# Kernel optimization log

Hardware: AMD Instinct MI355X
Metric: run time of the kernel (lower is better)

The kernel has to match this reference:

```python
import jax, jax.numpy as jnp
import numpy as np

HIDDEN = 2048
NUM_HEADS = 16
HEAD_DIM = HIDDEN // NUM_HEADS


def setup_inputs() -> dict:
    key = jax.random.key(0)
    k1, k2, k3 = jax.random.split(key, 3)
    hidden_states = jax.random.normal(k1, (4, 2048, HIDDEN), dtype=jnp.float32)
    # torch Linear weight is (out, in); y = x @ W.T. Store transposed (in, out).
    w_qkv = jax.random.normal(k2, (HIDDEN, 3 * HIDDEN), dtype=jnp.float32) * (HIDDEN ** -0.5)
    w_o = jax.random.normal(k3, (HIDDEN, HIDDEN), dtype=jnp.float32) * (HIDDEN ** -0.5)
    return {"hidden_states": hidden_states, "w_qkv": w_qkv, "w_o": w_o}


def reference(hidden_states, w_qkv, w_o):
    B, S, _ = hidden_states.shape
    qkv = hidden_states @ w_qkv  # (B, S, 3*HIDDEN)
    # Faithful to torch .view: row-major reshape straight to (B, H, S, 3*head_dim)
    qkv = qkv.reshape(B, NUM_HEADS, S, 3 * HEAD_DIM)
    q, k, v = jnp.split(qkv, 3, axis=-1)  # each (B, H, S, head_dim)
    scores = jnp.einsum('bhsd,bhtd->bhst', q, k) / (HEAD_DIM ** 0.5)
    probs = jax.nn.softmax(scores, axis=-1)
    attn = jnp.einsum('bhst,bhtd->bhsd', probs, v)  # (B, H, S, head_dim)
    # Faithful to torch .reshape(B, S, hidden) without transpose
    attn = attn.reshape(B, S, HIDDEN)
    return attn @ w_o
```

## Files before the change

kernel.cpp:

```cpp
#include <hip/hip_runtime.h>
#include <stdint.h>

#define DEVINL __device__ __forceinline__

typedef __attribute__((ext_vector_type(8))) __bf16 bf16x8;
typedef __attribute__((ext_vector_type(4))) float f32x4;
typedef __attribute__((ext_vector_type(16))) float f32x16;

static constexpr int HID  = 2048;
static constexpr int NQ   = 6144;
static constexpr int SEQ  = 2048;
static constexpr int NB   = 4;
static constexpr int MTOT = NB * SEQ;

DEVINL unsigned short f2bf(float f) {
  union { float f; uint32_t u; } x; x.f = f;
  uint32_t r = x.u + 0x7fffu + ((x.u >> 16) & 1u);
  return (unsigned short)(r >> 16);
}

typedef const __attribute__((address_space(1))) void gvoid_t;
typedef __attribute__((address_space(3))) void svoid_t;

DEVINL void gload_lds16(const void* g, void* s) {
  __builtin_amdgcn_global_load_lds((gvoid_t*)(uintptr_t)g,
                                   (svoid_t*)(uint32_t)(uintptr_t)s,
                                   16, 0, 0);
}


__global__ void k_cvt(const float* __restrict__ in, unsigned short* __restrict__ out, int n4) {
  int i = blockIdx.x * blockDim.x + threadIdx.x;
  if (i >= n4) return;
  float4 v = ((const float4*)in)[i];
  ushort4 o;
  o.x = f2bf(v.x); o.y = f2bf(v.y); o.z = f2bf(v.z); o.w = f2bf(v.w);
  ((ushort4*)out)[i] = o;
}

__global__ void k_transpose_cvt(const float* __restrict__ in, unsigned short* __restrict__ out,
                                int R, int C) {
  __shared__ float tile[32][33];
  int c0 = blockIdx.x * 32, r0 = blockIdx.y * 32;
  int tx = threadIdx.x & 31, ty = threadIdx.x >> 5;
  #pragma unroll
  for (int i = 0; i < 32; i += 8)
    tile[ty + i][tx] = in[(size_t)(r0 + ty + i) * C + (c0 + tx)];
  __syncthreads();
  #pragma unroll
  for (int i = 0; i < 32; i += 8)
    out[(size_t)(c0 + ty + i) * R + (r0 + tx)] = f2bf(tile[tx][ty + i]);
}


template <int OUT_BF16>
__global__ __launch_bounds__(256, 2) void k_gemm2(const unsigned short* __restrict__ A,
                                                  const unsigned short* __restrict__ BT,
                                                  void* __restrict__ Cout,
                                                  int M, int N, int K) {
  __shared__ unsigned short As[256 * 64];
  __shared__ unsigned short Bs[128 * 64];
  const int tid = threadIdx.x;
  const int w = tid >> 6, l = tid & 63;
  const int lane16 = l & 15, lgrp = l >> 4;
  const int bn = blockIdx.x, bm = blockIdx.y;
  const int srow = l >> 3;
  const int gslot = (l & 7) ^ (l >> 3);

  f32x4 acc[4][8] = {};

  for (int k0 = 0; k0 < K; k0 += 64) {
    #pragma unroll
    for (int i = 0; i < 8; ++i) {
      const int chunk = i * 4 + w;
      const int row = chunk * 8 + srow;
      gload_lds16(A + (size_t)(bm * 256 + row) * K + k0 + gslot * 8, As + chunk * 512);
    }
    #pragma unroll
    for (int i = 0; i < 4; ++i) {
      const int chunk = i * 4 + w;
      const int row = chunk * 8 + srow;
      gload_lds16(BT + (size_t)(bn * 128 + row) * K + k0 + gslot * 8, Bs + chunk * 512);
    }
    __syncthreads();

    #pragma unroll
    for (int kk = 0; kk < 2; ++kk) {
      bf16x8 af[4], bfr[8];
      #pragma unroll
      for (int mf = 0; mf < 4; ++mf) {
        const int row = w * 64 + mf * 16 + lane16;
        af[mf] = *(const bf16x8*)(As + row * 64 + (((kk * 4 + lgrp) ^ (row & 7)) * 8));
      }
      #pragma unroll
      for (int nf = 0; nf < 8; ++nf) {
        const int row = nf * 16 + lane16;
        bfr[nf] = *(const bf16x8*)(Bs + row * 64 + (((kk * 4 + lgrp) ^ (row & 7)) * 8));
      }
      #pragma unroll
      for (int mf = 0; mf < 4; ++mf)
        #pragma unroll
        for (int nf = 0; nf < 8; ++nf)
          acc[mf][nf] = __builtin_amdgcn_mfma_f32_16x16x32_bf16(af[mf], bfr[nf], acc[mf][nf], 0, 0, 0);
    }
    __syncthreads();
  }

  const size_t row0 = (size_t)bm * 256 + w * 64;
  const int col0 = bn * 128;
  #pragma unroll
  for (int mf = 0; mf < 4; ++mf) {
    #pragma unroll
    for (int nf = 0; nf < 8; ++nf) {
      const int col = col0 + nf * 16 + lane16;
      #pragma unroll
      for (int r = 0; r < 4; ++r) {
        const size_t row = row0 + mf * 16 + lgrp * 4 + r;
        if (OUT_BF16)
          ((unsigned short*)Cout)[row * N + col] = f2bf(acc[mf][nf][r]);
        else
          ((float*)Cout)[row * N + col] = acc[mf][nf][r];
      }
    }
  }
}

__global__ void k_build_vt(const unsigned short* __restrict__ QKV, unsigned short* __restrict__ Vt) {
  const int head = blockIdx.y;
  const int s_rel = blockIdx.x;
  const int b = head >> 4, h = head & 15;
  const int d = threadIdx.x;
  const unsigned short* src = QKV + (size_t)(b * SEQ + h * 128 + s_rel) * NQ + 256 + d;
  unsigned short vals[16];
  #pragma unroll
  for (int c1 = 0; c1 < 16; ++c1) vals[c1] = src[c1 * 384];
  unsigned short* dst = Vt + ((size_t)head * 128 + d) * SEQ + s_rel * 16;
  #pragma unroll
  for (int c1 = 0; c1 < 16; ++c1) dst[c1] = vals[c1];
}

__global__ __launch_bounds__(256, 2) void k_attn(const unsigned short* __restrict__ QKV,
                                                 const unsigned short* __restrict__ Vt,
                                                 unsigned short* __restrict__ ATT) {
  __shared__ unsigned short Ks[2][64 * 128];
  __shared__ unsigned short Vs[2][128 * 64];
  const int tid = threadIdx.x, w = tid >> 6, l = tid & 63;
  const int l32 = l & 31, hi = l >> 5;
  const int qt = blockIdx.x, head = blockIdx.y;
  const int b = head >> 4, h = head & 15;
  const float scale = 0.08838834764831845f;
  const float THR = 8.0f / 0.08838834764831845f;
  const int base_row = b * SEQ + h * 128;

  const int s = qt * 128 + w * 32 + l32;
  bf16x8 qf[8];
  {
    const unsigned short* qrow = QKV + (size_t)(base_row + (s >> 4)) * NQ + (s & 15) * 384;
    #pragma unroll
    for (int dsl = 0; dsl < 8; ++dsl)
      qf[dsl] = *(const bf16x8*)(qrow + dsl * 16 + hi * 8);
  }

  f32x16 oacc[4] = {};
  float mrun = -1e30f, lrun = 0.0f;

  #define STAGE_KV(bb, kv0)                                                              \
    {                                                                                    \
      _Pragma("unroll")                                                                  \
      for (int i = 0; i < 4; ++i) {                                                      \
        const int chunk = i * 4 + w;                                                     \
        const int r = chunk * 4 + (l >> 4);                                              \
        const int colsw = ((l & 15) ^ (r & 15)) * 8;                                     \
        gload_lds16(QKV + (size_t)(base_row + ((kv0) >> 4) + (r >> 4)) * NQ              \
                        + (r & 15) * 384 + 128 + colsw,                                  \
                    &Ks[bb][chunk * 512]);                                               \
      }                                                                                  \
      _Pragma("unroll")                                                                  \
      for (int i = 0; i < 4; ++i) {                                                      \
        const int chunk = i * 4 + w;                                                     \
        const int dr = chunk * 8 + (l >> 3);                                             \
        const int colsw = ((l & 7) ^ (dr & 7)) * 8;                                      \
        gload_lds16(Vt + ((size_t)head * 128 + dr) * SEQ + (kv0) + colsw,                \
                    &Vs[bb][chunk * 512]);                                               \
      }                                                                                  \
    }

  STAGE_KV(0, 0);
  __syncthreads();

  int buf = 0;
  for (int kv0 = 0; kv0 < SEQ; kv0 += 64) {
    if (kv0 + 64 < SEQ) STAGE_KV(buf ^ 1, kv0 + 64);

    f32x16 sacc[2] = {};
    __builtin_amdgcn_s_setprio(1);
    #pragma unroll
    for (int kvf = 0; kvf < 2; ++kvf) {
      const int row = kvf * 32 + l32;
      const unsigned short* kbase = &Ks[buf][row * 128];
      const int rs = (row & 15) << 3;
      #pragma unroll
      for (int dsl = 0; dsl < 8; ++dsl) {
        bf16x8 kf = *(const bf16x8*)(kbase + ((dsl * 16 + hi * 8) ^ rs));
        sacc[kvf] = __builtin_amdgcn_mfma_f32_32x32x16_bf16(kf, qf[dsl], sacc[kvf], 0, 0, 0);
      }
    }
    __builtin_amdgcn_s_setprio(0);

    float mx[16];
    #pragma unroll
    for (int r = 0; r < 16; ++r) mx[r] = fmaxf(sacc[0][r], sacc[1][r]);
    #pragma unroll
    for (int st = 8; st >= 1; st >>= 1)
      #pragma unroll
      for (int r = 0; r < st; ++r) mx[r] = fmaxf(mx[r], mx[r + st]);
    float pmax = fmaxf(mx[0], __shfl_xor(mx[0], 32));

    if (!__all(pmax - mrun <= THR)) {
      const float mnew = fmaxf(mrun, pmax);
      const float corr = __expf((mrun - mnew) * scale);
      #pragma unroll
      for (int df = 0; df < 4; ++df)
        #pragma unroll
        for (int r = 0; r < 16; ++r) oacc[df][r] *= corr;
      lrun *= corr;
      mrun = mnew;
    }

    float ps[16];
    #pragma unroll
    for (int r = 0; r < 16; ++r) {
      const float p0 = __expf((sacc[0][r] - mrun) * scale);
      const float p1 = __expf((sacc[1][r] - mrun) * scale);
      sacc[0][r] = p0; sacc[1][r] = p1;
      ps[r] = p0 + p1;
    }
    #pragma unroll
    for (int st = 8; st >= 1; st >>= 1)
      #pragma unroll
      for (int r = 0; r < st; ++r) ps[r] += ps[r + st];
    lrun += ps[0] + __shfl_xor(ps[0], 32);

    bf16x8 pf[4];
    #pragma unroll
    for (int f = 0; f < 2; ++f) {
      unsigned int c0, c1, c2, c3, c4, c5, c6, c7;
      asm("v_cvt_pk_bf16_f32 %0, %1, %2" : "=v"(c0) : "v"(sacc[f][0]),  "v"(sacc[f][1]));
      asm("v_cvt_pk_bf16_f32 %0, %1, %2" : "=v"(c1) : "v"(sacc[f][2]),  "v"(sacc[f][3]));
      asm("v_cvt_pk_bf16_f32 %0, %1, %2" : "=v"(c2) : "v"(sacc[f][4]),  "v"(sacc[f][5]));
      asm("v_cvt_pk_bf16_f32 %0, %1, %2" : "=v"(c3) : "v"(sacc[f][6]),  "v"(sacc[f][7]));
      asm("v_cvt_pk_bf16_f32 %0, %1, %2" : "=v"(c4) : "v"(sacc[f][8]),  "v"(sacc[f][9]));
      asm("v_cvt_pk_bf16_f32 %0, %1, %2" : "=v"(c5) : "v"(sacc[f][10]), "v"(sacc[f][11]));
      asm("v_cvt_pk_bf16_f32 %0, %1, %2" : "=v"(c6) : "v"(sacc[f][12]), "v"(sacc[f][13]));
      asm("v_cvt_pk_bf16_f32 %0, %1, %2" : "=v"(c7) : "v"(sacc[f][14]), "v"(sacc[f][15]));
      asm("v_permlane32_swap_b32 %0, %1" : "+v"(c0), "+v"(c2));
      asm("v_permlane32_swap_b32 %0, %1" : "+v"(c1), "+v"(c3));
      asm("v_permlane32_swap_b32 %0, %1" : "+v"(c4), "+v"(c6));
      asm("v_permlane32_swap_b32 %0, %1" : "+v"(c5), "+v"(c7));
      union { unsigned int u[4]; bf16x8 v; } u0, u1;
      u0.u[0] = c0; u0.u[1] = c1; u0.u[2] = c2; u0.u[3] = c3;
      u1.u[0] = c4; u1.u[1] = c5; u1.u[2] = c6; u1.u[3] = c7;
      pf[2 * f] = u0.v; pf[2 * f + 1] = u1.v;
    }

    __builtin_amdgcn_s_setprio(1);
    #pragma unroll
    for (int ks = 0; ks < 4; ++ks) {
      #pragma unroll
      for (int df = 0; df < 4; ++df) {
        const int row = df * 32 + l32;
        bf16x8 vf = *(const bf16x8*)(&Vs[buf][row * 64 + (((ks * 16 + hi * 8) ^ ((row & 7) << 3)))]);
        oacc[df] = __builtin_amdgcn_mfma_f32_32x32x16_bf16(vf, pf[ks], oacc[df], 0, 0, 0);
      }
    }
    __builtin_amdgcn_s_setprio(0);

    __syncthreads();
    buf ^= 1;
  }

  const float inv = 1.0f / lrun;
  unsigned short* orow = ATT + (size_t)(base_row + (s >> 4)) * HID + (s & 15) * 128;
  #pragma unroll
  for (int df = 0; df < 4; ++df) {
    #pragma unroll
    for (int k = 0; k < 4; ++k) {
      ushort4 o;
      o.x = f2bf(oacc[df][4 * k + 0] * inv);
      o.y = f2bf(oacc[df][4 * k + 1] * inv);
      o.z = f2bf(oacc[df][4 * k + 2] * inv);
      o.w = f2bf(oacc[df][4 * k + 3] * inv);
      *(ushort4*)(orow + df * 32 + 8 * k + 4 * hi) = o;
    }
  }
}


extern "C" void kernel_launch(void* const* d_in, const int* in_sizes, int n_in,
                              void* d_out, int out_size, void* d_ws, size_t ws_size,
                              hipStream_t stream) {
  const float* X    = (const float*)d_in[0];
  const float* Wqkv = (const float*)d_in[1];
  const float* Wo   = (const float*)d_in[2];
  float* OUT = (float*)d_out;

  char* ws = (char*)d_ws;
  constexpr size_t SZ_QKV   = (size_t)MTOT * NQ * 2;
  constexpr size_t SZ_XBF   = (size_t)MTOT * HID * 2;
  constexpr size_t SZ_WQKVT = (size_t)NQ * HID * 2;
  constexpr size_t SZ_WOT   = (size_t)HID * HID * 2;
  constexpr size_t SZ_VT    = (size_t)64 * 128 * SEQ * 2;
  unsigned short* QKV   = (unsigned short*)(ws);
  unsigned short* Xbf   = (unsigned short*)(ws + SZ_QKV);
  unsigned short* WqkvT = (unsigned short*)(ws + SZ_QKV + SZ_XBF);
  unsigned short* WoT   = (unsigned short*)(ws + SZ_QKV + SZ_XBF + SZ_WQKVT);
  unsigned short* Vt    = (unsigned short*)(ws + SZ_QKV + SZ_XBF + SZ_WQKVT + SZ_WOT);
  unsigned short* ATT   = (unsigned short*)(ws + SZ_QKV + SZ_XBF + SZ_WQKVT + SZ_WOT + SZ_VT);

  k_cvt<<<(MTOT * HID / 4 + 255) / 256, 256, 0, stream>>>(X, Xbf, MTOT * HID / 4);
  k_transpose_cvt<<<dim3(NQ / 32, HID / 32), 256, 0, stream>>>(Wqkv, WqkvT, HID, NQ);
  k_transpose_cvt<<<dim3(HID / 32, HID / 32), 256, 0, stream>>>(Wo, WoT, HID, HID);
  k_gemm2<1><<<dim3(NQ / 128, MTOT / 256), 256, 0, stream>>>(Xbf, WqkvT, QKV, MTOT, NQ, HID);
  k_build_vt<<<dim3(128, 64), 128, 0, stream>>>(QKV, Vt);
  k_attn<<<dim3(16, 64), 256, 0, stream>>>(QKV, Vt, ATT);
  k_gemm2<0><<<dim3(HID / 128, MTOT / 256), 256, 0, stream>>>(ATT, WoT, OUT, MTOT, HID, HID);
}
```

Before: 477.1 us.

## Load GEMM A operand directly to registers and fold softmax scale into Q

The GEMM kernel stops staging the A tile through shared memory. Each wave loads its own 64 rows of A straight from global memory into MFMA fragments, because no other wave reads those rows. This removes the A LDS traffic and frees shared memory, but the row-strided global loads are exposed to latency and are less coalesced. The QKV GEMM epilogue also multiplies Q columns by scale*log2(e), so the attention kernel can use a raw v_exp_f32 (exp2) without the per-element multiply.

```diff
diff --git a/kernel.cpp b/kernel.cpp
--- a/kernel.cpp
+++ b/kernel.cpp
@@ -18,6 +18,8 @@
   uint32_t r = x.u + 0x7fffu + ((x.u >> 16) & 1u);
   return (unsigned short)(r >> 16);
 }
+
+DEVINL float fexp2(float x) { float r; asm("v_exp_f32 %0, %1" : "=v"(r) : "v"(x)); return r; }
 
 typedef const __attribute__((address_space(1))) void gvoid_t;
 typedef __attribute__((address_space(3))) void svoid_t;
@@ -53,12 +55,11 @@
 }
 
 
-template <int OUT_BF16>
-__global__ __launch_bounds__(256, 2) void k_gemm2(const unsigned short* __restrict__ A,
+template <int OUT_BF16, int QSCALE>
+__global__ __launch_bounds__(256, 2) void k_gemm3(const unsigned short* __restrict__ A,
                                                   const unsigned short* __restrict__ BT,
                                                   void* __restrict__ Cout,
                                                   int M, int N, int K) {
-  __shared__ unsigned short As[256 * 64];
   __shared__ unsigned short Bs[128 * 64];
   const int tid = threadIdx.x;
   const int w = tid >> 6, l = tid & 63;
@@ -68,30 +69,26 @@
   const int gslot = (l & 7) ^ (l >> 3);
 
   f32x4 acc[4][8] = {};
+  const size_t abase = (size_t)(bm * 256 + w * 64 + lane16) * K;
 
   for (int k0 = 0; k0 < K; k0 += 64) {
-    #pragma unroll
-    for (int i = 0; i < 8; ++i) {
-      const int chunk = i * 4 + w;
-      const int row = chunk * 8 + srow;
-      gload_lds16(A + (size_t)(bm * 256 + row) * K + k0 + gslot * 8, As + chunk * 512);
-    }
     #pragma unroll
     for (int i = 0; i < 4; ++i) {
       const int chunk = i * 4 + w;
       const int row = chunk * 8 + srow;
       gload_lds16(BT + (size_t)(bn * 128 + row) * K + k0 + gslot * 8, Bs + chunk * 512);
     }
+    bf16x8 af[4][2];
+    #pragma unroll
+    for (int mf = 0; mf < 4; ++mf)
+      #pragma unroll
+      for (int kk = 0; kk < 2; ++kk)
+        af[mf][kk] = *(const bf16x8*)(A + abase + (size_t)mf * 16 * K + k0 + kk * 32 + lgrp * 8);
     __syncthreads();
 
     #pragma unroll
     for (int kk = 0; kk < 2; ++kk) {
-      bf16x8 af[4], bfr[8];
-      #pragma unroll
-      for (int mf = 0; mf < 4; ++mf) {
-        const int row = w * 64 + mf * 16 + lane16;
-        af[mf] = *(const bf16x8*)(As + row * 64 + (((kk * 4 + lgrp) ^ (row & 7)) * 8));
-      }
+      bf16x8 bfr[8];
       #pragma unroll
       for (int nf = 0; nf < 8; ++nf) {
         const int row = nf * 16 + lane16;
@@ -101,11 +98,12 @@
       for (int mf = 0; mf < 4; ++mf)
         #pragma unroll
         for (int nf = 0; nf < 8; ++nf)
-          acc[mf][nf] = __builtin_amdgcn_mfma_f32_16x16x32_bf16(af[mf], bfr[nf], acc[mf][nf], 0, 0, 0);
+          acc[mf][nf] = __builtin_amdgcn_mfma_f32_16x16x32_bf16(af[mf][kk], bfr[nf], acc[mf][nf], 0, 0, 0);
     }
     __syncthreads();
   }
 
+  const float qs = (QSCALE && (bn % 3 == 0)) ? 0.12751744f : 1.0f;
   const size_t row0 = (size_t)bm * 256 + w * 64;
   const int col0 = bn * 128;
   #pragma unroll
@@ -117,7 +115,7 @@
       for (int r = 0; r < 4; ++r) {
         const size_t row = row0 + mf * 16 + lgrp * 4 + r;
         if (OUT_BF16)
-          ((unsigned short*)Cout)[row * N + col] = f2bf(acc[mf][nf][r]);
+          ((unsigned short*)Cout)[row * N + col] = f2bf(acc[mf][nf][r] * qs);
         else
           ((float*)Cout)[row * N + col] = acc[mf][nf][r];
       }
@@ -148,8 +146,7 @@
   const int l32 = l & 31, hi = l >> 5;
   const int qt = blockIdx.x, head = blockIdx.y;
   const int b = head >> 4, h = head & 15;
-  const float scale = 0.08838834764831845f;
-  const float THR = 8.0f / 0.08838834764831845f;
+  const float THR = 11.5415603f;
   const int base_row = b * SEQ + h * 128;
 
   const int s = qt * 128 + w * 32 + l32;
@@ -218,7 +215,7 @@
 
     if (!__all(pmax - mrun <= THR)) {
       const float mnew = fmaxf(mrun, pmax);
-      const float corr = __expf((mrun - mnew) * scale);
+      const float corr = fexp2(mrun - mnew);
       #pragma unroll
       for (int df = 0; df < 4; ++df)
         #pragma unroll
@@ -230,8 +227,8 @@
     float ps[16];
     #pragma unroll
     for (int r = 0; r < 16; ++r) {
-      const float p0 = __expf((sacc[0][r] - mrun) * scale);
-      const float p1 = __expf((sacc[1][r] - mrun) * scale);
+      const float p0 = fexp2(sacc[0][r] - mrun);
+      const float p1 = fexp2(sacc[1][r] - mrun);
       sacc[0][r] = p0; sacc[1][r] = p1;
       ps[r] = p0 + p1;
     }
@@ -320,8 +317,8 @@
   k_cvt<<<(MTOT * HID / 4 + 255) / 256, 256, 0, stream>>>(X, Xbf, MTOT * HID / 4);
   k_transpose_cvt<<<dim3(NQ / 32, HID / 32), 256, 0, stream>>>(Wqkv, WqkvT, HID, NQ);
   k_transpose_cvt<<<dim3(HID / 32, HID / 32), 256, 0, stream>>>(Wo, WoT, HID, HID);
-  k_gemm2<1><<<dim3(NQ / 128, MTOT / 256), 256, 0, stream>>>(Xbf, WqkvT, QKV, MTOT, NQ, HID);
+  k_gemm3<1, 1><<<dim3(NQ / 128, MTOT / 256), 256, 0, stream>>>(Xbf, WqkvT, QKV, MTOT, NQ, HID);
   k_build_vt<<<dim3(128, 64), 128, 0, stream>>>(QKV, Vt);
   k_attn<<<dim3(16, 64), 256, 0, stream>>>(QKV, Vt, ATT);
-  k_gemm2<0><<<dim3(HID / 128, MTOT / 256), 256, 0, stream>>>(ATT, WoT, OUT, MTOT, HID, HID);
-}
+  k_gemm3<0, 0><<<dim3(HID / 128, MTOT / 256), 256, 0, stream>>>(ATT, WoT, OUT, MTOT, HID, HID);
+}
```

Result: slower. 516.1 us (+8.2%).

## Fold softmax scale into QKV GEMM epilogue, use exp2, tile V transpose via LDS

Applied to the files above, without the earlier changes.

The QKV GEMM epilogue now scales the Q columns (every third 128-column block) by scale*log2(e), so the attention kernel can call the raw v_exp_f32 (exp2) directly with no per-element multiply. The rescale threshold is adjusted to match. The V-transpose kernel is rewritten to stage 128x128 tiles in LDS, replacing strided scalar gathers with 16-byte coalesced loads and vector stores. The trade-off is that Q is rounded to bf16 after scaling, and the epilogue has a block-index-dependent multiply.

```diff
diff --git a/kernel.cpp b/kernel.cpp
--- a/kernel.cpp
+++ b/kernel.cpp
@@ -18,6 +18,8 @@
   uint32_t r = x.u + 0x7fffu + ((x.u >> 16) & 1u);
   return (unsigned short)(r >> 16);
 }
+
+DEVINL float fexp2(float x) { float r; asm("v_exp_f32 %0, %1" : "=v"(r) : "v"(x)); return r; }
 
 typedef const __attribute__((address_space(1))) void gvoid_t;
 typedef __attribute__((address_space(3))) void svoid_t;
@@ -53,7 +55,7 @@
 }
 
 
-template <int OUT_BF16>
+template <int OUT_BF16, int QSCALE>
 __global__ __launch_bounds__(256, 2) void k_gemm2(const unsigned short* __restrict__ A,
                                                   const unsigned short* __restrict__ BT,
                                                   void* __restrict__ Cout,
@@ -106,6 +108,7 @@
     __syncthreads();
   }
 
+  const float qs = (QSCALE && (bn % 3 == 0)) ? 0.12751744f : 1.0f;
   const size_t row0 = (size_t)bm * 256 + w * 64;
   const int col0 = bn * 128;
   #pragma unroll
@@ -117,7 +120,7 @@
       for (int r = 0; r < 4; ++r) {
         const size_t row = row0 + mf * 16 + lgrp * 4 + r;
         if (OUT_BF16)
-          ((unsigned short*)Cout)[row * N + col] = f2bf(acc[mf][nf][r]);
+          ((unsigned short*)Cout)[row * N + col] = f2bf(acc[mf][nf][r] * qs);
         else
           ((float*)Cout)[row * N + col] = acc[mf][nf][r];
       }
@@ -125,18 +128,38 @@
   }
 }
 
-__global__ void k_build_vt(const unsigned short* __restrict__ QKV, unsigned short* __restrict__ Vt) {
+__global__ __launch_bounds__(256, 2) void k_build_vt2(const unsigned short* __restrict__ QKV,
+                                                      unsigned short* __restrict__ Vt) {
+  __shared__ unsigned short lt[128][136];
   const int head = blockIdx.y;
-  const int s_rel = blockIdx.x;
+  const int tblk = blockIdx.x;
   const int b = head >> 4, h = head & 15;
-  const int d = threadIdx.x;
-  const unsigned short* src = QKV + (size_t)(b * SEQ + h * 128 + s_rel) * NQ + 256 + d;
-  unsigned short vals[16];
-  #pragma unroll
-  for (int c1 = 0; c1 < 16; ++c1) vals[c1] = src[c1 * 384];
-  unsigned short* dst = Vt + ((size_t)head * 128 + d) * SEQ + s_rel * 16;
-  #pragma unroll
-  for (int c1 = 0; c1 < 16; ++c1) dst[c1] = vals[c1];
+  const int base_row = b * SEQ + h * 128;
+  const int tid = threadIdx.x;
+
+  #pragma unroll
+  for (int it = 0; it < 8; ++it) {
+    const int idx = it * 256 + tid;
+    const int tt = idx >> 4, dgrp = idx & 15;
+    const uint4 v = *(const uint4*)(QKV + (size_t)(base_row + tblk * 8 + (tt >> 4)) * NQ
+                                        + (tt & 15) * 384 + 256 + dgrp * 8);
+    *(uint4*)(&lt[tt][dgrp * 8]) = v;
+  }
+  __syncthreads();
+
+  #pragma unroll
+  for (int it = 0; it < 8; ++it) {
+    const int idx = it * 256 + tid;
+    const int d = idx >> 4, tgrp = idx & 15;
+    ushort4 a, bq;
+    a.x = lt[tgrp * 8 + 0][d]; a.y = lt[tgrp * 8 + 1][d];
+    a.z = lt[tgrp * 8 + 2][d]; a.w = lt[tgrp * 8 + 3][d];
+    bq.x = lt[tgrp * 8 + 4][d]; bq.y = lt[tgrp * 8 + 5][d];
+    bq.z = lt[tgrp * 8 + 6][d]; bq.w = lt[tgrp * 8 + 7][d];
+    unsigned short* dst = Vt + ((size_t)head * 128 + d) * SEQ + tblk * 128 + tgrp * 8;
+    *(ushort4*)(dst) = a;
+    *(ushort4*)(dst + 4) = bq;
+  }
 }
 
 __global__ __launch_bounds__(256, 2) void k_attn(const unsigned short* __restrict__ QKV,
@@ -148,8 +171,7 @@
   const int l32 = l & 31, hi = l >> 5;
   const int qt = blockIdx.x, head = blockIdx.y;
   const int b = head >> 4, h = head & 15;
-  const float scale = 0.08838834764831845f;
-  const float THR = 8.0f / 0.08838834764831845f;
+  const float THR = 11.5415603f;
   const int base_row = b * SEQ + h * 128;
 
   const int s = qt * 128 + w * 32 + l32;
@@ -218,7 +240,7 @@
 
     if (!__all(pmax - mrun <= THR)) {
       const float mnew = fmaxf(mrun, pmax);
-      const float corr = __expf((mrun - mnew) * scale);
+      const float corr = fexp2(mrun - mnew);
       #pragma unroll
       for (int df = 0; df < 4; ++df)
         #pragma unroll
@@ -230,8 +252,8 @@
     float ps[16];
     #pragma unroll
     for (int r = 0; r < 16; ++r) {
-      const float p0 = __expf((sacc[0][r] - mrun) * scale);
-      const float p1 = __expf((sacc[1][r] - mrun) * scale);
+      const float p0 = fexp2(sacc[0][r] - mrun);
+      const float p1 = fexp2(sacc[1][r] - mrun);
       sacc[0][r] = p0; sacc[1][r] = p1;
       ps[r] = p0 + p1;
     }
@@ -320,8 +342,8 @@
   k_cvt<<<(MTOT * HID / 4 + 255) / 256, 256, 0, stream>>>(X, Xbf, MTOT * HID / 4);
   k_transpose_cvt<<<dim3(NQ / 32, HID / 32), 256, 0, stream>>>(Wqkv, WqkvT, HID, NQ);
   k_transpose_cvt<<<dim3(HID / 32, HID / 32), 256, 0, stream>>>(Wo, WoT, HID, HID);
-  k_gemm2<1><<<dim3(NQ / 128, MTOT / 256), 256, 0, stream>>>(Xbf, WqkvT, QKV, MTOT, NQ, HID);
-  k_build_vt<<<dim3(128, 64), 128, 0, stream>>>(QKV, Vt);
+  k_gemm2<1, 1><<<dim3(NQ / 128, MTOT / 256), 256, 0, stream>>>(Xbf, WqkvT, QKV, MTOT, NQ, HID);
+  k_build_vt2<<<dim3(16, 64), 256, 0, stream>>>(QKV, Vt);
   k_attn<<<dim3(16, 64), 256, 0, stream>>>(QKV, Vt, ATT);
-  k_gemm2<0><<<dim3(HID / 128, MTOT / 256), 256, 0, stream>>>(ATT, WoT, OUT, MTOT, HID, HID);
-}
+  k_gemm2<0, 0><<<dim3(HID / 128, MTOT / 256), 256, 0, stream>>>(ATT, WoT, OUT, MTOT, HID, HID);
+}
```

Measured after the change: 467.0 us. 2.1% less time.
